# Kernel optimization log

Measured on AMD Instinct MI355X. Metric: run time of the kernel, lower is better.

The kernel has to match this reference:

```python
import jax, jax.numpy as jnp
import numpy as np

N_LAYERS = 4
BN_EPS = 1e-5


def setup_inputs() -> dict:
    key = jax.random.key(0)
    ks = jax.random.split(key, 10)
    N, E, F, H = 50000, 600000, 128, 128
    x = jax.random.normal(ks[0], (N, F), dtype=jnp.float32)
    edge_index = jax.random.randint(ks[1], (2, E), 0, N, dtype=jnp.int64)
    s = 0.05  # small init to keep deep ReLU stack numerically tame
    return {
        "x": x,
        "edge_index": edge_index,
        # stacked params for the 4 GINConv MLPs (num_features == hidden)
        "conv_w1": jax.random.normal(ks[2], (N_LAYERS, F, H), dtype=jnp.float32) * s,
        "conv_b1": jnp.zeros((N_LAYERS, H), dtype=jnp.float32),
        "conv_gamma": jnp.ones((N_LAYERS, H), dtype=jnp.float32),
        "conv_beta": jnp.zeros((N_LAYERS, H), dtype=jnp.float32),
        "conv_w2": jax.random.normal(ks[3], (N_LAYERS, H, H), dtype=jnp.float32) * s,
        "conv_b2": jnp.zeros((N_LAYERS, H), dtype=jnp.float32),
        "fc1_w": jax.random.normal(ks[4], (H, H), dtype=jnp.float32) * s,
        "fc1_b": jnp.zeros((H,), dtype=jnp.float32),
        "fc2_w": jax.random.normal(ks[5], (H, 1), dtype=jnp.float32) * s,
        "fc2_b": jnp.zeros((1,), dtype=jnp.float32),
    }


def _batchnorm(h, gamma, beta):
    # training-mode BatchNorm1d: batch stats over the node axis, biased variance
    mean = jnp.mean(h, axis=0, keepdims=True)
    var = jnp.mean(jnp.square(h - mean), axis=0, keepdims=True)
    return (h - mean) * jax.lax.rsqrt(var + BN_EPS) * gamma + beta


def _gin_layer(x, src, dst, w1, b1, gamma, beta, w2, b2):
    n = x.shape[0]
    # GIN sum aggregation with eps=0: (1+eps)*x_i + sum_{j->i} x_j
    agg = x + jax.ops.segment_sum(x[src], dst, num_segments=n)
    h = jax.nn.relu(agg @ w1 + b1)
    h = _batchnorm(h, gamma, beta)
    return jax.nn.relu(h @ w2 + b2)


def reference(x, edge_index, conv_w1, conv_b1, conv_gamma, conv_beta,
              conv_w2, conv_b2, fc1_w, fc1_b, fc2_w, fc2_b):
    src, dst = edge_index[0], edge_index[1]
    h = x
    for l in range(N_LAYERS):
        h = _gin_layer(h, src, dst, conv_w1[l], conv_b1[l], conv_gamma[l],
                       conv_beta[l], conv_w2[l], conv_b2[l])
    h = jax.nn.relu(h @ fc1_w + fc1_b)
    return h @ fc2_w + fc2_b  # [N, 1]
```

## Files before the change

kernel.cpp:

```cpp
#include <hip/hip_runtime.h>

constexpr int FEAT = 128;

typedef __attribute__((ext_vector_type(8))) _Float16 f16x8;
typedef __attribute__((ext_vector_type(4))) float f32x4;

__device__ inline unsigned int halfpair(float a, float b) {
  unsigned short ua = __builtin_bit_cast(unsigned short, (_Float16)a);
  unsigned short ub = __builtin_bit_cast(unsigned short, (_Float16)b);
  return (unsigned int)ua | ((unsigned int)ub << 16);
}
__device__ inline unsigned short halfr(float a) {
  return __builtin_bit_cast(unsigned short, (_Float16)a);
}
__device__ inline float2 halfup(unsigned int u) {
  _Float16 lo = __builtin_bit_cast(_Float16, (unsigned short)(u & 0xffffu));
  _Float16 hi = __builtin_bit_cast(_Float16, (unsigned short)(u >> 16));
  return make_float2((float)lo, (float)hi);
}

__device__ __host__ inline int kperm(int k) {
  return ((k >> 5) << 5) + (((k >> 2) & 3) << 3) + (((k >> 4) & 1) << 2) + (k & 3);
}


__global__ void count_kernel(const int* __restrict__ dst, int* __restrict__ deg, int E) {
  int e = blockIdx.x * blockDim.x + threadIdx.x;
  if (e < E) atomicAdd(&deg[dst[e]], 1);
}

__global__ __launch_bounds__(256) void scan1_kernel(const int* __restrict__ in,
                                                    int* __restrict__ bsum, int n) {
  int base = blockIdx.x * 1024 + threadIdx.x * 4;
  int s = 0;
  if (base + 3 < n) {
    int4 v = *(const int4*)(in + base);
    s = v.x + v.y + v.z + v.w;
  } else {
#pragma unroll
    for (int j = 0; j < 4; j++)
      if (base + j < n) s += in[base + j];
  }
#pragma unroll
  for (int off = 1; off < 64; off <<= 1) s += __shfl_xor(s, off);
  __shared__ int ws[4];
  int lane = threadIdx.x & 63, wid = threadIdx.x >> 6;
  if (lane == 0) ws[wid] = s;
  __syncthreads();
  if (threadIdx.x == 0) bsum[blockIdx.x] = ws[0] + ws[1] + ws[2] + ws[3];
}

__global__ __launch_bounds__(64) void scan2_kernel(int* __restrict__ bsum, int nb) {
  int t = threadIdx.x;
  int v = (t < nb) ? bsum[t] : 0;
  int s = v;
#pragma unroll
  for (int off = 1; off < 64; off <<= 1) {
    int u = __shfl_up(s, off);
    if (t >= off) s += u;
  }
  if (t < nb) bsum[t] = s - v;
}

__global__ __launch_bounds__(256) void scan3_kernel(const int* __restrict__ in,
                                                    const int* __restrict__ boff,
                                                    int* __restrict__ out,
                                                    int* __restrict__ out2, int n) {
  int t = threadIdx.x;
  int base = blockIdx.x * 1024 + t * 4;
  int v0 = 0, v1 = 0, v2 = 0, v3 = 0;
  if (base + 3 < n) {
    int4 v = *(const int4*)(in + base);
    v0 = v.x; v1 = v.y; v2 = v.z; v3 = v.w;
  } else {
    if (base + 0 < n) v0 = in[base + 0];
    if (base + 1 < n) v1 = in[base + 1];
    if (base + 2 < n) v2 = in[base + 2];
  }
  int ts = v0 + v1 + v2 + v3;
  int s = ts;
  int lane = t & 63, wid = t >> 6;
#pragma unroll
  for (int off = 1; off < 64; off <<= 1) {
    int u = __shfl_up(s, off);
    if (lane >= off) s += u;
  }
  __shared__ int ws[4];
  if (lane == 63) ws[wid] = s;
  __syncthreads();
  int cross = 0;
#pragma unroll
  for (int i = 0; i < 4; i++)
    if (i < wid) cross += ws[i];
  int excl = boff[blockIdx.x] + cross + (s - ts);
  int o0 = excl, o1 = o0 + v0, o2 = o1 + v1, o3 = o2 + v2;
  if (base + 3 < n) {
    *(int4*)(out + base) = make_int4(o0, o1, o2, o3);
    *(int4*)(out2 + base) = make_int4(o0, o1, o2, o3);
  } else {
    if (base + 0 < n) { out[base + 0] = o0; out2[base + 0] = o0; }
    if (base + 1 < n) { out[base + 1] = o1; out2[base + 1] = o1; }
    if (base + 2 < n) { out[base + 2] = o2; out2[base + 2] = o2; }
  }
}

__global__ void fill_kernel(const int* __restrict__ src, const int* __restrict__ dst,
                            int* __restrict__ cursor, int* __restrict__ col, int E) {
  int e = blockIdx.x * blockDim.x + threadIdx.x;
  if (e < E) {
    int p = atomicAdd(&cursor[dst[e]], 1);
    col[p] = src[e];
  }
}


__global__ void convert_kernel(const float* __restrict__ x, unsigned short* __restrict__ xb,
                               int n4) {
  int idx = blockIdx.x * blockDim.x + threadIdx.x;
  if (idx >= n4) return;
  float4 v = ((const float4*)x)[idx];
  uint2 o;
  o.x = halfpair(v.x, v.y);
  o.y = halfpair(v.z, v.w);
  ((uint2*)xb)[idx] = o;
}


__global__ void wconv_kernel(const float* __restrict__ w1, const float* __restrict__ fc1w,
                             unsigned short* __restrict__ dst) {
  int idx = blockIdx.x * blockDim.x + threadIdx.x;
  if (idx >= 5 * FEAT * FEAT) return;
  int m = idx >> 14;
  int r = idx & (FEAT * FEAT - 1);
  int k = r >> 7, n = r & 127;
  float v = (m < 4) ? w1[idx] : fc1w[r];
  int p = kperm(k);
  int slot = p >> 3, e = p & 7;
  dst[m * FEAT * FEAT + n * FEAT + ((slot ^ (n & 7)) << 3) + e] = halfr(v);
}


__global__ void agg_kernel(const unsigned short* __restrict__ x, const int* __restrict__ rowptr,
                           const int* __restrict__ col, unsigned short* __restrict__ agg, int N) {
  int gid = blockIdx.x * blockDim.x + threadIdx.x;
  int wid = gid >> 6;
  int lane = threadIdx.x & 63;
  int node = wid * 4 + (lane >> 4);
  if (node >= N) return;
  int ln = lane & 15;
  const uint4* xr = (const uint4*)x;
  uint4 s = xr[(size_t)node * 16 + ln];
  float2 t0 = halfup(s.x), t1 = halfup(s.y), t2 = halfup(s.z), t3 = halfup(s.w);
  float a0 = t0.x, a1 = t0.y, a2 = t1.x, a3 = t1.y;
  float a4 = t2.x, a5 = t2.y, a6 = t3.x, a7 = t3.y;
  float b0 = 0.f, b1 = 0.f, b2 = 0.f, b3 = 0.f;
  float b4 = 0.f, b5 = 0.f, b6 = 0.f, b7 = 0.f;
  int e0 = rowptr[node], e1 = rowptr[node + 1];
  int e = e0;
  for (; e + 3 < e1; e += 4) {
    int c0 = col[e], c1 = col[e + 1], c2 = col[e + 2], c3 = col[e + 3];
    uint4 v = xr[(size_t)c0 * 16 + ln];
    uint4 u = xr[(size_t)c1 * 16 + ln];
    uint4 w = xr[(size_t)c2 * 16 + ln];
    uint4 z = xr[(size_t)c3 * 16 + ln];
    float2 f;
    f = halfup(v.x); a0 += f.x; a1 += f.y;
    f = halfup(v.y); a2 += f.x; a3 += f.y;
    f = halfup(v.z); a4 += f.x; a5 += f.y;
    f = halfup(v.w); a6 += f.x; a7 += f.y;
    f = halfup(u.x); b0 += f.x; b1 += f.y;
    f = halfup(u.y); b2 += f.x; b3 += f.y;
    f = halfup(u.z); b4 += f.x; b5 += f.y;
    f = halfup(u.w); b6 += f.x; b7 += f.y;
    f = halfup(w.x); a0 += f.x; a1 += f.y;
    f = halfup(w.y); a2 += f.x; a3 += f.y;
    f = halfup(w.z); a4 += f.x; a5 += f.y;
    f = halfup(w.w); a6 += f.x; a7 += f.y;
    f = halfup(z.x); b0 += f.x; b1 += f.y;
    f = halfup(z.y); b2 += f.x; b3 += f.y;
    f = halfup(z.z); b4 += f.x; b5 += f.y;
    f = halfup(z.w); b6 += f.x; b7 += f.y;
  }
  for (; e < e1; e++) {
    uint4 v = xr[(size_t)col[e] * 16 + ln];
    float2 f;
    f = halfup(v.x); a0 += f.x; a1 += f.y;
    f = halfup(v.y); a2 += f.x; a3 += f.y;
    f = halfup(v.z); a4 += f.x; a5 += f.y;
    f = halfup(v.w); a6 += f.x; a7 += f.y;
  }
  a0 += b0; a1 += b1; a2 += b2; a3 += b3;
  a4 += b4; a5 += b5; a6 += b6; a7 += b7;
  uint4 o;
  o.x = halfpair(a0, a1);
  o.y = halfpair(a2, a3);
  o.z = halfpair(a4, a5);
  o.w = halfpair(a6, a7);
  ((uint4*)agg)[(size_t)node * 16 + ln] = o;
}


__global__ __launch_bounds__(256) void gemm_kernel(
    const unsigned short* __restrict__ A, const unsigned short* __restrict__ Wimg,
    const float* __restrict__ bias, unsigned short* __restrict__ C,
    float* __restrict__ pS, float* __restrict__ pQ, int N, int doStats) {
  __shared__ unsigned short Al[FEAT * FEAT];
  __shared__ unsigned short Wl[FEAT * FEAT];
  __shared__ float ls[FEAT], lq[FEAT];

  int tx = threadIdx.x;
  int row0 = blockIdx.x * FEAT;
  if (tx < FEAT) { ls[tx] = 0.f; lq[tx] = 0.f; }

#pragma unroll
  for (int i = 0; i < 8; i++) {
    int idx = tx + i * 256;
    ((uint4*)Wl)[idx] = ((const uint4*)Wimg)[idx];
  }
#pragma unroll
  for (int i = 0; i < 16; i++) {
    int idx = tx + i * 256;
    int r = idx >> 5;
    int c = idx & 31;
    uint2 v = make_uint2(0u, 0u);
    if (row0 + r < N) v = ((const uint2*)(A + (size_t)(row0 + r) * FEAT))[c];
    int k0 = c << 2;
    int p0 = ((k0 >> 5) << 5) + (((k0 >> 2) & 3) << 3) + (((k0 >> 4) & 1) << 2);
    int slot = p0 >> 3, half4 = (p0 >> 2) & 1;
    *(uint2*)&Al[r * FEAT + ((slot ^ (r & 7)) << 3) + (half4 << 2)] = v;
  }
  __syncthreads();

  int w = tx >> 6;
  int l = tx & 63;
  int llo = l & 15, lhi = l >> 4;
  int wr = (w >> 1) * 64, wc = (w & 1) * 64;

  f32x4 acc[4][4];
#pragma unroll
  for (int mi = 0; mi < 4; mi++)
#pragma unroll
    for (int nj = 0; nj < 4; nj++) acc[mi][nj] = (f32x4)(0.f);

#pragma unroll
  for (int s = 0; s < 4; s++) {
    f16x8 af[4], wf[4];
#pragma unroll
    for (int mi = 0; mi < 4; mi++) {
      int row = wr + mi * 16 + llo;
      int base = row * FEAT + ((((s << 2) + lhi) ^ (row & 7)) << 3);
      af[mi] = *(const f16x8*)&Al[base];
    }
#pragma unroll
    for (int nj = 0; nj < 4; nj++) {
      int n = wc + nj * 16 + llo;
      int base = n * FEAT + ((((s << 2) + lhi) ^ (n & 7)) << 3);
      wf[nj] = *(const f16x8*)&Wl[base];
    }
#pragma unroll
    for (int mi = 0; mi < 4; mi++)
#pragma unroll
      for (int nj = 0; nj < 4; nj++)
        acc[mi][nj] = __builtin_amdgcn_mfma_f32_16x16x32_f16(wf[nj], af[mi], acc[mi][nj], 0, 0, 0);
  }

#pragma unroll
  for (int nj = 0; nj < 4; nj++) {
    int colb = wc + nj * 16 + lhi * 4;
    float4 bb = *(const float4*)&bias[colb];
    float ps[4] = {0.f, 0.f, 0.f, 0.f}, pq[4] = {0.f, 0.f, 0.f, 0.f};
#pragma unroll
    for (int mi = 0; mi < 4; mi++) {
      int row = row0 + wr + mi * 16 + llo;
      f32x4 v = acc[mi][nj];
      float v0 = fmaxf(v[0] + bb.x, 0.f);
      float v1 = fmaxf(v[1] + bb.y, 0.f);
      float v2 = fmaxf(v[2] + bb.z, 0.f);
      float v3 = fmaxf(v[3] + bb.w, 0.f);
      if (row < N) {
        *(uint2*)&C[(size_t)row * FEAT + colb] = make_uint2(halfpair(v0, v1), halfpair(v2, v3));
        ps[0] += v0; ps[1] += v1; ps[2] += v2; ps[3] += v3;
        pq[0] += v0 * v0; pq[1] += v1 * v1; pq[2] += v2 * v2; pq[3] += v3 * v3;
      }
    }
    if (doStats) {
#pragma unroll
      for (int r = 0; r < 4; r++) {
        float s2 = ps[r], q2 = pq[r];
#pragma unroll
        for (int off = 1; off < 16; off <<= 1) {
          s2 += __shfl_xor(s2, off);
          q2 += __shfl_xor(q2, off);
        }
        if (llo == 0) {
          atomicAdd(&ls[colb + r], s2);
          atomicAdd(&lq[colb + r], q2);
        }
      }
    }
  }
  if (doStats) {
    __syncthreads();
    if (tx < FEAT) {
      pS[(size_t)blockIdx.x * FEAT + tx] = ls[tx];
      pQ[(size_t)blockIdx.x * FEAT + tx] = lq[tx];
    }
  }
}


__global__ __launch_bounds__(64) void stats_kernel(
    const float* __restrict__ pS, const float* __restrict__ pQ, int nblk,
    const float* __restrict__ gamma, const float* __restrict__ beta,
    float* __restrict__ scf, float* __restrict__ shf, int N) {
  int c = blockIdx.x;
  int ln = threadIdx.x;
  float s = 0.f, q = 0.f;
  for (int b = ln; b < nblk; b += 64) {
    s += pS[(size_t)b * FEAT + c];
    q += pQ[(size_t)b * FEAT + c];
  }
#pragma unroll
  for (int off = 32; off; off >>= 1) {
    s += __shfl_xor(s, off);
    q += __shfl_xor(q, off);
  }
  if (ln == 0) {
    float invN = 1.0f / (float)N;
    float mean = s * invN;
    float var = q * invN - mean * mean;
    float rstd = rsqrtf(var + 1e-5f);
    float scale = gamma[c] * rstd;
    scf[c] = scale;
    shf[c] = beta[c] - mean * scale;
  }
}


__global__ __launch_bounds__(128) void fold2_kernel(
    const float* __restrict__ scf, const float* __restrict__ shf,
    const float* __restrict__ w2, const float* __restrict__ b2,
    unsigned short* __restrict__ w2f, float* __restrict__ b2f) {
  __shared__ float red[FEAT];
  int c = blockIdx.x;
  int k = threadIdx.x;
  float wv = w2[k * FEAT + c];
  int p = kperm(k);
  int slot = p >> 3, e = p & 7;
  w2f[c * FEAT + ((slot ^ (c & 7)) << 3) + e] = halfr(scf[k] * wv);
  red[k] = shf[k] * wv;
  __syncthreads();
#pragma unroll
  for (int off = 64; off > 0; off >>= 1) {
    if (k < off) red[k] += red[k + off];
    __syncthreads();
  }
  if (k == 0) b2f[c] = b2[c] + red[0];
}


__global__ void fc2_kernel(const unsigned short* __restrict__ h, const float* __restrict__ w,
                           const float* __restrict__ b, float* __restrict__ out, int N) {
  int gid = blockIdx.x * blockDim.x + threadIdx.x;
  int node = gid >> 6;
  if (node >= N) return;
  int lane = threadIdx.x & 63;
  float2 hv = halfup(((const unsigned int*)h)[(size_t)node * 64 + lane]);
  float2 wv = ((const float2*)w)[lane];
  float s = hv.x * wv.x + hv.y * wv.y;
#pragma unroll
  for (int off = 32; off; off >>= 1) s += __shfl_xor(s, off);
  if (lane == 0) out[node] = s + b[0];
}


extern "C" void kernel_launch(void* const* d_in, const int* in_sizes, int n_in,
                              void* d_out, int out_size, void* d_ws, size_t ws_size,
                              hipStream_t stream) {
  const float* x     = (const float*)d_in[0];
  const int*   ei    = (const int*)d_in[1];
  const float* w1    = (const float*)d_in[2];
  const float* b1    = (const float*)d_in[3];
  const float* gamma = (const float*)d_in[4];
  const float* beta  = (const float*)d_in[5];
  const float* w2    = (const float*)d_in[6];
  const float* b2    = (const float*)d_in[7];
  const float* fc1w  = (const float*)d_in[8];
  const float* fc1b  = (const float*)d_in[9];
  const float* fc2w  = (const float*)d_in[10];
  const float* fc2b  = (const float*)d_in[11];
  float* out = (float*)d_out;

  int N = in_sizes[0] / FEAT;
  int E = in_sizes[1] / 2;
  const int* srcI = ei;
  const int* dstI = ei + E;

  int gemmBlocks = (N + FEAT - 1) / FEAT;
  int n = N + 1;
  int nb = (n + 1023) / 1024;

  size_t Nf = (size_t)N * FEAT;
  unsigned short* H = (unsigned short*)d_ws;
  unsigned short* G = H + Nf;
  unsigned short* wimg = G + Nf;
  unsigned short* w2f = wimg + 5 * FEAT * FEAT;
  float* b2f = (float*)(w2f + FEAT * FEAT);
  float* scf = b2f + FEAT;
  float* shf = scf + FEAT;
  float* pS = shf + FEAT;
  float* pQ = pS + (size_t)gemmBlocks * FEAT;
  int* deg = (int*)(pQ + (size_t)gemmBlocks * FEAT);
  int* rowptr = deg + ((n + 3) & ~3);
  int* cursor = rowptr + ((n + 3) & ~3);
  int* bsum = cursor + ((n + 3) & ~3);
  int* col = bsum + 64;

  hipMemsetAsync(deg, 0, n * sizeof(int), stream);
  count_kernel<<<(E + 255) / 256, 256, 0, stream>>>(dstI, deg, E);
  scan1_kernel<<<nb, 256, 0, stream>>>(deg, bsum, n);
  scan2_kernel<<<1, 64, 0, stream>>>(bsum, nb);
  scan3_kernel<<<nb, 256, 0, stream>>>(deg, bsum, rowptr, cursor, n);
  fill_kernel<<<(E + 255) / 256, 256, 0, stream>>>(srcI, dstI, cursor, col, E);

  int n4 = (int)(Nf / 4);
  convert_kernel<<<(n4 + 255) / 256, 256, 0, stream>>>(x, H, n4);
  wconv_kernel<<<(5 * FEAT * FEAT + 255) / 256, 256, 0, stream>>>(w1, fc1w, wimg);

  int aggBlocks = (int)((((size_t)(N + 3) / 4) * 64 + 255) / 256);
  int fc2Blocks = (int)(((size_t)N * 64 + 255) / 256);

  for (int l = 0; l < 4; l++) {
    agg_kernel<<<aggBlocks, 256, 0, stream>>>(H, rowptr, col, G, N);
    gemm_kernel<<<gemmBlocks, 256, 0, stream>>>(G, wimg + (size_t)l * FEAT * FEAT,
                                                b1 + (size_t)l * FEAT, G, pS, pQ, N, 1);
    stats_kernel<<<FEAT, 64, 0, stream>>>(pS, pQ, gemmBlocks, gamma + (size_t)l * FEAT,
                                          beta + (size_t)l * FEAT, scf, shf, N);
    fold2_kernel<<<FEAT, FEAT, 0, stream>>>(scf, shf, w2 + (size_t)l * FEAT * FEAT,
                                            b2 + (size_t)l * FEAT, w2f, b2f);
    gemm_kernel<<<gemmBlocks, 256, 0, stream>>>(G, w2f, b2f, H, nullptr, nullptr, N, 0);
  }

  gemm_kernel<<<gemmBlocks, 256, 0, stream>>>(H, wimg + (size_t)4 * FEAT * FEAT, fc1b, G,
                                              nullptr, nullptr, N, 0);
  fc2_kernel<<<fc2Blocks, 256, 0, stream>>>(G, fc2w, fc2b, out, N);
}
```

Baseline: 425.2 us.

## Fuse BN stats and weight folding into GEMM via last-block reduction, fuse fc2

The GEMM now runs with 512 threads (8 waves, each covering a 64x32 tile). The first GEMM of each layer uses an atomic counter so the last block reduces the per-block BN partials and folds scale and shift into W2 and b2. This removes the separate stats and fold2 launches. The final fc1 GEMM applies fc2 in its epilogue, so the fc1 activations are never written and the fc2 kernel is dropped. The cost is a serial tail in the last block, plus extra threadfences and atomics.

New measurement: 720.1 us. +69.4%, slower.

```diff
diff --git a/kernel.cpp b/kernel.cpp
--- a/kernel.cpp
+++ b/kernel.cpp
@@ -200,26 +200,32 @@
 }
 
 
-__global__ __launch_bounds__(256) void gemm_kernel(
+__global__ __launch_bounds__(512, 4) void gemm_kernel(
     const unsigned short* __restrict__ A, const unsigned short* __restrict__ Wimg,
     const float* __restrict__ bias, unsigned short* __restrict__ C,
-    float* __restrict__ pS, float* __restrict__ pQ, int N, int doStats) {
+    float* __restrict__ pS, float* __restrict__ pQ, int N, int mode,
+    const float* __restrict__ gamma, const float* __restrict__ beta,
+    const float* __restrict__ w2, const float* __restrict__ b2,
+    unsigned short* __restrict__ w2f, float* __restrict__ b2f, int* __restrict__ cntL,
+    const float* __restrict__ fc2w, const float* __restrict__ fc2b,
+    float* __restrict__ outp) {
   __shared__ unsigned short Al[FEAT * FEAT];
   __shared__ unsigned short Wl[FEAT * FEAT];
-  __shared__ float ls[FEAT], lq[FEAT];
+  __shared__ float ls[FEAT], lq[FEAT], red[FEAT];
+  __shared__ int amLast;
 
   int tx = threadIdx.x;
   int row0 = blockIdx.x * FEAT;
-  if (tx < FEAT) { ls[tx] = 0.f; lq[tx] = 0.f; }
-
+  if (tx < FEAT) { ls[tx] = 0.f; lq[tx] = 0.f; red[tx] = 0.f; }
+
+#pragma unroll
+  for (int i = 0; i < 4; i++) {
+    int idx = tx + i * 512;
+    ((uint4*)Wl)[idx] = ((const uint4*)Wimg)[idx];
+  }
 #pragma unroll
   for (int i = 0; i < 8; i++) {
-    int idx = tx + i * 256;
-    ((uint4*)Wl)[idx] = ((const uint4*)Wimg)[idx];
-  }
-#pragma unroll
-  for (int i = 0; i < 16; i++) {
-    int idx = tx + i * 256;
+    int idx = tx + i * 512;
     int r = idx >> 5;
     int c = idx & 31;
     uint2 v = make_uint2(0u, 0u);
@@ -234,38 +240,69 @@
   int w = tx >> 6;
   int l = tx & 63;
   int llo = l & 15, lhi = l >> 4;
-  int wr = (w >> 1) * 64, wc = (w & 1) * 64;
-
-  f32x4 acc[4][4];
+  int wr = (w >> 2) * 64;
+  int wc = (w & 3) * 32;
+
+  f32x4 acc[4][2];
 #pragma unroll
   for (int mi = 0; mi < 4; mi++)
 #pragma unroll
-    for (int nj = 0; nj < 4; nj++) acc[mi][nj] = (f32x4)(0.f);
+    for (int nj = 0; nj < 2; nj++) acc[mi][nj] = (f32x4)(0.f);
 
 #pragma unroll
   for (int s = 0; s < 4; s++) {
-    f16x8 af[4], wf[4];
+    f16x8 af[4], wf[2];
 #pragma unroll
     for (int mi = 0; mi < 4; mi++) {
       int row = wr + mi * 16 + llo;
-      int base = row * FEAT + ((((s << 2) + lhi) ^ (row & 7)) << 3);
-      af[mi] = *(const f16x8*)&Al[base];
-    }
-#pragma unroll
-    for (int nj = 0; nj < 4; nj++) {
+      af[mi] = *(const f16x8*)&Al[row * FEAT + ((((s << 2) + lhi) ^ (row & 7)) << 3)];
+    }
+#pragma unroll
+    for (int nj = 0; nj < 2; nj++) {
       int n = wc + nj * 16 + llo;
-      int base = n * FEAT + ((((s << 2) + lhi) ^ (n & 7)) << 3);
-      wf[nj] = *(const f16x8*)&Wl[base];
+      wf[nj] = *(const f16x8*)&Wl[n * FEAT + ((((s << 2) + lhi) ^ (n & 7)) << 3)];
     }
 #pragma unroll
     for (int mi = 0; mi < 4; mi++)
 #pragma unroll
-      for (int nj = 0; nj < 4; nj++)
+      for (int nj = 0; nj < 2; nj++)
         acc[mi][nj] = __builtin_amdgcn_mfma_f32_16x16x32_f16(wf[nj], af[mi], acc[mi][nj], 0, 0, 0);
   }
 
-#pragma unroll
-  for (int nj = 0; nj < 4; nj++) {
+  if (mode == 2) {
+    float pr[4] = {0.f, 0.f, 0.f, 0.f};
+#pragma unroll
+    for (int nj = 0; nj < 2; nj++) {
+      int colb = wc + nj * 16 + lhi * 4;
+      float4 bb = *(const float4*)&bias[colb];
+      float4 fw = *(const float4*)&fc2w[colb];
+#pragma unroll
+      for (int mi = 0; mi < 4; mi++) {
+        f32x4 v = acc[mi][nj];
+        float v0 = fmaxf(v[0] + bb.x, 0.f);
+        float v1 = fmaxf(v[1] + bb.y, 0.f);
+        float v2 = fmaxf(v[2] + bb.z, 0.f);
+        float v3 = fmaxf(v[3] + bb.w, 0.f);
+        pr[mi] += v0 * fw.x + v1 * fw.y + v2 * fw.z + v3 * fw.w;
+      }
+    }
+#pragma unroll
+    for (int mi = 0; mi < 4; mi++) {
+      float r = pr[mi];
+      r += __shfl_xor(r, 16);
+      r += __shfl_xor(r, 32);
+      if (lhi == 0) atomicAdd(&red[wr + mi * 16 + llo], r);
+    }
+    __syncthreads();
+    if (tx < FEAT) {
+      int row = row0 + tx;
+      if (row < N) outp[row] = red[tx] + fc2b[0];
+    }
+    return;
+  }
+
+#pragma unroll
+  for (int nj = 0; nj < 2; nj++) {
     int colb = wc + nj * 16 + lhi * 4;
     float4 bb = *(const float4*)&bias[colb];
     float ps[4] = {0.f, 0.f, 0.f, 0.f}, pq[4] = {0.f, 0.f, 0.f, 0.f};
@@ -283,7 +320,7 @@
         pq[0] += v0 * v0; pq[1] += v1 * v1; pq[2] += v2 * v2; pq[3] += v3 * v3;
       }
     }
-    if (doStats) {
+    if (mode == 1) {
 #pragma unroll
       for (int r = 0; r < 4; r++) {
         float s2 = ps[r], q2 = pq[r];
@@ -299,78 +336,58 @@
       }
     }
   }
-  if (doStats) {
+
+  if (mode == 1) {
     __syncthreads();
     if (tx < FEAT) {
       pS[(size_t)blockIdx.x * FEAT + tx] = ls[tx];
       pQ[(size_t)blockIdx.x * FEAT + tx] = lq[tx];
     }
-  }
-}
-
-
-__global__ __launch_bounds__(64) void stats_kernel(
-    const float* __restrict__ pS, const float* __restrict__ pQ, int nblk,
-    const float* __restrict__ gamma, const float* __restrict__ beta,
-    float* __restrict__ scf, float* __restrict__ shf, int N) {
-  int c = blockIdx.x;
-  int ln = threadIdx.x;
-  float s = 0.f, q = 0.f;
-  for (int b = ln; b < nblk; b += 64) {
-    s += pS[(size_t)b * FEAT + c];
-    q += pQ[(size_t)b * FEAT + c];
-  }
-#pragma unroll
-  for (int off = 32; off; off >>= 1) {
-    s += __shfl_xor(s, off);
-    q += __shfl_xor(q, off);
-  }
-  if (ln == 0) {
-    float invN = 1.0f / (float)N;
-    float mean = s * invN;
-    float var = q * invN - mean * mean;
-    float rstd = rsqrtf(var + 1e-5f);
-    float scale = gamma[c] * rstd;
-    scf[c] = scale;
-    shf[c] = beta[c] - mean * scale;
-  }
-}
-
-
-__global__ __launch_bounds__(128) void fold2_kernel(
-    const float* __restrict__ scf, const float* __restrict__ shf,
-    const float* __restrict__ w2, const float* __restrict__ b2,
-    unsigned short* __restrict__ w2f, float* __restrict__ b2f) {
-  __shared__ float red[FEAT];
-  int c = blockIdx.x;
-  int k = threadIdx.x;
-  float wv = w2[k * FEAT + c];
-  int p = kperm(k);
-  int slot = p >> 3, e = p & 7;
-  w2f[c * FEAT + ((slot ^ (c & 7)) << 3) + e] = halfr(scf[k] * wv);
-  red[k] = shf[k] * wv;
-  __syncthreads();
-#pragma unroll
-  for (int off = 64; off > 0; off >>= 1) {
-    if (k < off) red[k] += red[k + off];
+    __threadfence();
     __syncthreads();
-  }
-  if (k == 0) b2f[c] = b2[c] + red[0];
-}
-
-
-__global__ void fc2_kernel(const unsigned short* __restrict__ h, const float* __restrict__ w,
-                           const float* __restrict__ b, float* __restrict__ out, int N) {
-  int gid = blockIdx.x * blockDim.x + threadIdx.x;
-  int node = gid >> 6;
-  if (node >= N) return;
-  int lane = threadIdx.x & 63;
-  float2 hv = halfup(((const unsigned int*)h)[(size_t)node * 64 + lane]);
-  float2 wv = ((const float2*)w)[lane];
-  float s = hv.x * wv.x + hv.y * wv.y;
-#pragma unroll
-  for (int off = 32; off; off >>= 1) s += __shfl_xor(s, off);
-  if (lane == 0) out[node] = s + b[0];
+    if (tx == 0) amLast = (atomicAdd(cntL, 1) == (int)gridDim.x - 1);
+    __syncthreads();
+    if (amLast) {
+      __threadfence();
+      int nblk = gridDim.x;
+      float* sred = (float*)Wl;
+      float* qred = sred + 512;
+      int c = tx & 127, q4 = tx >> 7;
+      float S = 0.f, Q = 0.f;
+      for (int b = q4; b < nblk; b += 4) {
+        S += pS[(size_t)b * FEAT + c];
+        Q += pQ[(size_t)b * FEAT + c];
+      }
+      sred[q4 * 128 + c] = S;
+      qred[q4 * 128 + c] = Q;
+      __syncthreads();
+      float* sc = (float*)Al;
+      float* sh = sc + 128;
+      if (q4 == 0) {
+        float Ss = sred[c] + sred[128 + c] + sred[256 + c] + sred[384 + c];
+        float Qs = qred[c] + qred[128 + c] + qred[256 + c] + qred[384 + c];
+        float invN = 1.0f / (float)N;
+        float mean = Ss * invN;
+        float var = Qs * invN - mean * mean;
+        float rstd = rsqrtf(var + 1e-5f);
+        float scale = gamma[c] * rstd;
+        sc[c] = scale;
+        sh[c] = beta[c] - mean * scale;
+      }
+      __syncthreads();
+      float bacc = 0.f;
+      for (int k = q4 * 32; k < q4 * 32 + 32; k++) {
+        float wv = w2[k * FEAT + c];
+        int p = kperm(k);
+        int slot = p >> 3, e = p & 7;
+        w2f[c * FEAT + ((slot ^ (c & 7)) << 3) + e] = halfr(sc[k] * wv);
+        bacc += sh[k] * wv;
+      }
+      sred[q4 * 128 + c] = bacc;
+      __syncthreads();
+      if (q4 == 0) b2f[c] = b2[c] + sred[c] + sred[128 + c] + sred[256 + c] + sred[384 + c];
+    }
+  }
 }
 
 
@@ -406,17 +423,16 @@
   unsigned short* wimg = G + Nf;
   unsigned short* w2f = wimg + 5 * FEAT * FEAT;
   float* b2f = (float*)(w2f + FEAT * FEAT);
-  float* scf = b2f + FEAT;
-  float* shf = scf + FEAT;
-  float* pS = shf + FEAT;
+  float* pS = b2f + FEAT;
   float* pQ = pS + (size_t)gemmBlocks * FEAT;
-  int* deg = (int*)(pQ + (size_t)gemmBlocks * FEAT);
+  int* cnt = (int*)(pQ + (size_t)gemmBlocks * FEAT);
+  int* deg = cnt + 8;
   int* rowptr = deg + ((n + 3) & ~3);
   int* cursor = rowptr + ((n + 3) & ~3);
   int* bsum = cursor + ((n + 3) & ~3);
   int* col = bsum + 64;
 
-  hipMemsetAsync(deg, 0, n * sizeof(int), stream);
+  hipMemsetAsync(cnt, 0, (8 + n) * sizeof(int), stream);
   count_kernel<<<(E + 255) / 256, 256, 0, stream>>>(dstI, deg, E);
   scan1_kernel<<<nb, 256, 0, stream>>>(deg, bsum, n);
   scan2_kernel<<<1, 64, 0, stream>>>(bsum, nb);
@@ -428,20 +444,21 @@
   wconv_kernel<<<(5 * FEAT * FEAT + 255) / 256, 256, 0, stream>>>(w1, fc1w, wimg);
 
   int aggBlocks = (int)((((size_t)(N + 3) / 4) * 64 + 255) / 256);
-  int fc2Blocks = (int)(((size_t)N * 64 + 255) / 256);
 
   for (int l = 0; l < 4; l++) {
     agg_kernel<<<aggBlocks, 256, 0, stream>>>(H, rowptr, col, G, N);
-    gemm_kernel<<<gemmBlocks, 256, 0, stream>>>(G, wimg + (size_t)l * FEAT * FEAT,
-                                                b1 + (size_t)l * FEAT, G, pS, pQ, N, 1);
-    stats_kernel<<<FEAT, 64, 0, stream>>>(pS, pQ, gemmBlocks, gamma + (size_t)l * FEAT,
-                                          beta + (size_t)l * FEAT, scf, shf, N);
-    fold2_kernel<<<FEAT, FEAT, 0, stream>>>(scf, shf, w2 + (size_t)l * FEAT * FEAT,
-                                            b2 + (size_t)l * FEAT, w2f, b2f);
-    gemm_kernel<<<gemmBlocks, 256, 0, stream>>>(G, w2f, b2f, H, nullptr, nullptr, N, 0);
-  }
-
-  gemm_kernel<<<gemmBlocks, 256, 0, stream>>>(H, wimg + (size_t)4 * FEAT * FEAT, fc1b, G,
-                                              nullptr, nullptr, N, 0);
-  fc2_kernel<<<fc2Blocks, 256, 0, stream>>>(G, fc2w, fc2b, out, N);
-}
+    gemm_kernel<<<gemmBlocks, 512, 0, stream>>>(
+        G, wimg + (size_t)l * FEAT * FEAT, b1 + (size_t)l * FEAT, G, pS, pQ, N, 1,
+        gamma + (size_t)l * FEAT, beta + (size_t)l * FEAT, w2 + (size_t)l * FEAT * FEAT,
+        b2 + (size_t)l * FEAT, w2f, b2f, cnt + l, nullptr, nullptr, nullptr);
+    gemm_kernel<<<gemmBlocks, 512, 0, stream>>>(
+        G, w2f, b2f, H, nullptr, nullptr, N, 0,
+        nullptr, nullptr, nullptr, nullptr, nullptr, nullptr, nullptr,
+        nullptr, nullptr, nullptr);
+  }
+
+  gemm_kernel<<<gemmBlocks, 512, 0, stream>>>(
+      H, wimg + (size_t)4 * FEAT * FEAT, fc1b, nullptr, nullptr, nullptr, N, 2,
+      nullptr, nullptr, nullptr, nullptr, nullptr, nullptr, nullptr,
+      fc2w, fc2b, out);
+}
```
